# Performance work log

Hardware: AMD Instinct MI355X
Metric: run time of the kernel (lower is better)

The kernel has to match this reference:

```python
import jax, jax.numpy as jnp
import numpy as np
from jax import lax

NUM_CLASSES = 21
MAX_OUT = 5          # max_output_size in tf.image.non_max_suppression
IOU_THR = 0.5        # NMS_IOU_THRESHOLD
CONF_THR = 0.5       # CONFIDENCE_THRESHOLD
NEG = -1e9           # stand-in for -inf score (suppressed / background)


def setup_inputs() -> dict:
    key = jax.random.key(0)
    k1, k2, k3 = jax.random.split(key, 3)
    B, N, C = 128, 8732, NUM_CLASSES
    logits = jax.random.normal(k1, (B, N, 4 + C), dtype=jnp.float32)
    # default boxes in corner format [ymin, xmin, ymax, xmax], valid geometry
    ctr = jax.random.uniform(k2, (N, 2), dtype=jnp.float32)                 # cy, cx
    sz = jax.random.uniform(k3, (N, 2), dtype=jnp.float32, minval=0.05, maxval=0.3)  # h, w
    default_boxes = jnp.clip(
        jnp.concatenate([ctr - sz / 2, ctr + sz / 2], axis=-1), 0.0, 1.0)
    return {"logits": logits, "default_boxes": default_boxes}


def _decode(loc, db):
    # db: [N,4] corners -> center/size (matches get_offset's tf.stack)
    cy = (db[:, 2] + db[:, 0]) / 2
    cx = (db[:, 3] + db[:, 1]) / 2
    h = db[:, 2] - db[:, 0]
    w = db[:, 3] - db[:, 1]
    # loc: [B,N,4] = (dy, dx, dh, dw)
    ncy = loc[..., 0] * h + cy
    ncx = loc[..., 1] * w + cx
    nh = jnp.exp(loc[..., 2]) * h
    nw = jnp.exp(loc[..., 3]) * w
    boxes = jnp.stack(
        [ncy - nh / 2, ncx - nw / 2, ncy + nh / 2, ncx + nw / 2], axis=-1)
    return jnp.clip(boxes, 0.0, 1.0)


def _iou_one_vs_all(box, boxes):
    # box [4], boxes [N,4], corner format
    tl = jnp.maximum(box[:2], boxes[:, :2])
    br = jnp.minimum(box[2:], boxes[:, 2:])
    wh = jnp.maximum(br - tl, 0.0)
    inter = wh[:, 0] * wh[:, 1]
    a1 = (box[2] - box[0]) * (box[3] - box[1])
    a2 = (boxes[:, 2] - boxes[:, 0]) * (boxes[:, 3] - boxes[:, 1])
    return inter / (a1 + a2 - inter + 1e-12)


def _nms_single(boxes, scores, classes_f):
    # boxes [N,4], scores [N] (background already set to NEG), classes_f [N] float
    def step(s, _):
        i = jnp.argmax(s)
        sc = s[i]
        b = boxes[i]
        valid = sc > CONF_THR  # score_threshold in tf NMS
        iou = _iou_one_vs_all(b, boxes)
        s = jnp.where(iou > IOU_THR, NEG, s)  # suppresses i too (IoU=1)
        return s, (b, classes_f[i], sc, valid)

    _, (bs, cs, ss, vs) = lax.scan(step, scores, None, length=MAX_OUT)
    # pad invalid slots with zeros (TF returns variable-length; we use fixed 5 + zero pad)
    bs = jnp.where(vs[:, None], bs, 0.0)
    cs = jnp.where(vs, cs, 0.0)
    ss = jnp.where(vs, ss, 0.0)
    return bs, cs[:, None], ss[:, None]  # [5,4], [5,1], [5,1]


def reference(logits, default_boxes):
    boxes = _decode(logits[..., :4], default_boxes)          # [B,N,4]
    probs = jax.nn.softmax(logits[..., 4:], axis=-1)         # [B,N,C]
    scores = jnp.max(probs, axis=-1)                          # [B,N]
    classes = jnp.argmax(probs, axis=-1)                      # [B,N] int
    # boolean_mask(classes != 0) expressed as score = -inf for background
    scores_eff = jnp.where(classes != 0, scores, NEG)
    det_b, det_c, det_s = jax.vmap(_nms_single)(
        boxes, scores_eff, classes.astype(jnp.float32))
    # pack detection_boxes / detection_classes / detection_scores -> [B,5,6]
    return jnp.concatenate([det_b, det_c, det_s], axis=-1)
```

## Files before the change

### kernel.cpp

```cpp
#include <hip/hip_runtime.h>

#define NEG (-1e9f)
constexpr int NCLS   = 21;
constexpr int NBOX   = 8732;
constexpr int MAXOUT = 5;
constexpr int CAP    = NBOX;
constexpr float IOU_THR  = 0.5f;
constexpr float CONF_THR = 0.5f;

__device__ __forceinline__ void process_box(
        const float* __restrict__ v,
        int idx,
        const float4* __restrict__ dbox4,
        float4* __restrict__ cand,
        int* __restrict__ cnt) {
    const int n = idx % NBOX;
    const int b = idx / NBOX;

    float4 db = dbox4[n];
    float cy = (db.z + db.x) * 0.5f;
    float cx = (db.w + db.y) * 0.5f;
    float h  = db.z - db.x;
    float w  = db.w - db.y;
    float ncy = v[0] * h + cy;
    float ncx = v[1] * w + cx;
    float nh  = expf(v[2]) * h;
    float nw  = expf(v[3]) * w;
    float y1 = fminf(fmaxf(ncy - nh * 0.5f, 0.f), 1.f);
    float x1 = fminf(fmaxf(ncx - nw * 0.5f, 0.f), 1.f);
    float y2 = fminf(fmaxf(ncy + nh * 0.5f, 0.f), 1.f);
    float x2 = fminf(fmaxf(ncx + nw * 0.5f, 0.f), 1.f);

    float m = v[4];
    int am = 0;
#pragma unroll
    for (int j = 1; j < NCLS; j++) {
        float x = v[4 + j];
        if (x > m) { m = x; am = j; }
    }
    float sum = 0.f;
#pragma unroll
    for (int j = 0; j < NCLS; j++) sum += expf(v[4 + j] - m);
    float score = 1.0f / sum;

    if (am != 0 && score > CONF_THR) {
        int p = atomicAdd(&cnt[b], 1);
        if (p < CAP) {
            float4* c = cand + ((long long)b * CAP + p) * 2;
            c[0] = make_float4(y1, x1, y2, x2);
            c[1] = make_float4(score, (float)am, (float)n, 0.f);
        }
    }
}

__global__ __launch_bounds__(128) void decode_kernel(
        const float* __restrict__ logits,
        const float4* __restrict__ dbox4,
        float4* __restrict__ cand,
        int* __restrict__ cnt,
        int BN) {
    const int g = (blockIdx.x * 128 + threadIdx.x) * 4;
    if (g >= BN) return;

    if (g + 3 < BN) {
        const float4* f4 = (const float4*)(logits + (long long)g * 25);
        float v[100];
#pragma unroll
        for (int k = 0; k < 25; k++) {
            float4 r = f4[k];
            v[4 * k + 0] = r.x; v[4 * k + 1] = r.y;
            v[4 * k + 2] = r.z; v[4 * k + 3] = r.w;
        }
#pragma unroll
        for (int j = 0; j < 4; j++)
            process_box(v + 25 * j, g + j, dbox4, cand, cnt);
    } else {
        for (int j = 0; j < 4 && g + j < BN; j++) {
            const float* L = logits + (long long)(g + j) * 25;
            float v[25];
#pragma unroll
            for (int k = 0; k < 25; k++) v[k] = L[k];
            process_box(v, g + j, dbox4, cand, cnt);
        }
    }
}

__global__ __launch_bounds__(64) void nms_kernel(
        const float4* __restrict__ cand,
        const int* __restrict__ cnt,
        float* __restrict__ out) {
    const int b    = blockIdx.x;
    const int lane = threadIdx.x;
    __shared__ float s_sc[CAP];
    __shared__ float s_id[CAP];

    const int M = min(cnt[b], CAP);
    const float4* cb = cand + (long long)b * CAP * 2;
    float* o = out + (long long)b * MAXOUT * 6;

    for (int i = lane; i < M; i += 64) {
        float4 mrec = cb[i * 2 + 1];
        s_sc[i] = mrec.x;
        s_id[i] = mrec.z;
    }

    int k = 0;
    for (; k < MAXOUT; k++) {
        float bv = -INFINITY, boid = 3.0e38f;
        int bi = -1;
        for (int i = lane; i < M; i += 64) {
            float v = s_sc[i], oid = s_id[i];
            if (v > bv || (v == bv && oid < boid)) { bv = v; boid = oid; bi = i; }
        }
        for (int mm = 32; mm >= 1; mm >>= 1) {
            float v2 = __shfl_xor(bv,   mm, 64);
            float o2 = __shfl_xor(boid, mm, 64);
            int   i2 = __shfl_xor(bi,   mm, 64);
            if (v2 > bv || (v2 == bv && o2 < boid)) { bv = v2; boid = o2; bi = i2; }
        }
        if (bi < 0 || !(bv > CONF_THR)) break;

        float4 sb = cb[bi * 2];
        if (lane == 0) {
            float4 mm2 = cb[bi * 2 + 1];
            o[k * 6 + 0] = sb.x; o[k * 6 + 1] = sb.y;
            o[k * 6 + 2] = sb.z; o[k * 6 + 3] = sb.w;
            o[k * 6 + 4] = mm2.y; o[k * 6 + 5] = bv;
        }

        float a1 = (sb.z - sb.x) * (sb.w - sb.y);
        for (int i = lane; i < M; i += 64) {
            float4 c = cb[i * 2];
            float tly = fmaxf(sb.x, c.x);
            float tlx = fmaxf(sb.y, c.y);
            float bry = fminf(sb.z, c.z);
            float brx = fminf(sb.w, c.w);
            float wh0 = fmaxf(bry - tly, 0.f);
            float wh1 = fmaxf(brx - tlx, 0.f);
            float inter = wh0 * wh1;
            float a2 = (c.z - c.x) * (c.w - c.y);
            float iou = inter / (a1 + a2 - inter + 1e-12f);
            if (iou > IOU_THR) s_sc[i] = NEG;
        }
    }
    for (int j = k * 6 + lane; j < MAXOUT * 6; j += 64) o[j] = 0.f;
}

extern "C" void kernel_launch(void* const* d_in, const int* in_sizes, int n_in,
                              void* d_out, int out_size, void* d_ws, size_t ws_size,
                              hipStream_t stream) {
    const float* logits = (const float*)d_in[0];
    const float4* dbox4 = (const float4*)d_in[1];
    float* out          = (float*)d_out;

    const int N  = in_sizes[1] / 4;
    const int B  = in_sizes[0] / (N * 25);
    const int BN = B * N;

    int* cnt = (int*)d_ws;
    float4* cand = (float4*)((char*)d_ws + (((size_t)B * sizeof(int) + 15) & ~(size_t)15));

    hipMemsetAsync(cnt, 0, (size_t)B * sizeof(int), stream);
    const int nthreads = (BN + 3) / 4;
    decode_kernel<<<(nthreads + 127) / 128, 128, 0, stream>>>(logits, dbox4, cand, cnt, BN);
    nms_kernel<<<B, 64, 0, stream>>>(cand, cnt, out);
}
```

Before: 192.9 us.

## Split decode into score pass and sparse gather pass for candidates

```diff
diff --git a/kernel.cpp b/kernel.cpp
--- a/kernel.cpp
+++ b/kernel.cpp
@@ -8,79 +8,110 @@
 constexpr float IOU_THR  = 0.5f;
 constexpr float CONF_THR = 0.5f;
 
-__device__ __forceinline__ void process_box(
-        const float* __restrict__ v,
-        int idx,
+__global__ __launch_bounds__(128) void score_kernel(
+        const float* __restrict__ logits,
+        float4* __restrict__ score_out,
+        int BN) {
+    const int q = blockIdx.x * 128 + threadIdx.x;
+    const int g = q * 4;
+    if (g >= BN) return;
+
+    float s_res[4];
+    if (g + 3 < BN) {
+        const float4* f4 = (const float4*)(logits + (long long)g * 25);
+        float v[100];
+#pragma unroll
+        for (int k = 0; k < 25; k++) {
+            float4 r = f4[k];
+            v[4 * k + 0] = r.x; v[4 * k + 1] = r.y;
+            v[4 * k + 2] = r.z; v[4 * k + 3] = r.w;
+        }
+#pragma unroll
+        for (int j = 0; j < 4; j++) {
+            const float* L = v + 25 * j;
+            float m = L[4];
+            int am = 0;
+#pragma unroll
+            for (int jj = 1; jj < NCLS; jj++) {
+                float x = L[4 + jj];
+                if (x > m) { m = x; am = jj; }
+            }
+            float sum = 0.f;
+#pragma unroll
+            for (int jj = 0; jj < NCLS; jj++) sum += expf(L[4 + jj] - m);
+            float score = 1.0f / sum;
+            s_res[j] = (am != 0) ? score : NEG;
+        }
+    } else {
+#pragma unroll
+        for (int j = 0; j < 4; j++) {
+            if (g + j >= BN) { s_res[j] = NEG; continue; }
+            const float* L = logits + (long long)(g + j) * 25;
+            float m = L[4];
+            int am = 0;
+            for (int jj = 1; jj < NCLS; jj++) {
+                float x = L[4 + jj];
+                if (x > m) { m = x; am = jj; }
+            }
+            float sum = 0.f;
+            for (int jj = 0; jj < NCLS; jj++) sum += expf(L[4 + jj] - m);
+            float score = 1.0f / sum;
+            s_res[j] = (am != 0) ? score : NEG;
+        }
+    }
+    score_out[q] = make_float4(s_res[0], s_res[1], s_res[2], s_res[3]);
+}
+
+__global__ __launch_bounds__(128) void gather_kernel(
+        const float* __restrict__ logits,
         const float4* __restrict__ dbox4,
+        const float4* __restrict__ score_in,
         float4* __restrict__ cand,
-        int* __restrict__ cnt) {
-    const int n = idx % NBOX;
-    const int b = idx / NBOX;
-
-    float4 db = dbox4[n];
-    float cy = (db.z + db.x) * 0.5f;
-    float cx = (db.w + db.y) * 0.5f;
-    float h  = db.z - db.x;
-    float w  = db.w - db.y;
-    float ncy = v[0] * h + cy;
-    float ncx = v[1] * w + cx;
-    float nh  = expf(v[2]) * h;
-    float nw  = expf(v[3]) * w;
-    float y1 = fminf(fmaxf(ncy - nh * 0.5f, 0.f), 1.f);
-    float x1 = fminf(fmaxf(ncx - nw * 0.5f, 0.f), 1.f);
-    float y2 = fminf(fmaxf(ncy + nh * 0.5f, 0.f), 1.f);
-    float x2 = fminf(fmaxf(ncx + nw * 0.5f, 0.f), 1.f);
-
-    float m = v[4];
-    int am = 0;
-#pragma unroll
-    for (int j = 1; j < NCLS; j++) {
-        float x = v[4 + j];
-        if (x > m) { m = x; am = j; }
-    }
-    float sum = 0.f;
-#pragma unroll
-    for (int j = 0; j < NCLS; j++) sum += expf(v[4 + j] - m);
-    float score = 1.0f / sum;
-
-    if (am != 0 && score > CONF_THR) {
+        int* __restrict__ cnt,
+        int BN) {
+    const int q = blockIdx.x * 128 + threadIdx.x;
+    const int g = q * 4;
+    if (g >= BN) return;
+    float4 s4 = score_in[q];
+    float sc[4] = { s4.x, s4.y, s4.z, s4.w };
+
+#pragma unroll
+    for (int j = 0; j < 4; j++) {
+        const int idx = g + j;
+        if (idx >= BN) continue;
+        const float score = sc[j];
+        if (!(score > CONF_THR)) continue;
+
+        const int n = idx % NBOX;
+        const int b = idx / NBOX;
+        const float* L = logits + (long long)idx * 25;
+
+        float m = L[4];
+        int am = 0;
+        for (int jj = 1; jj < NCLS; jj++) {
+            float x = L[4 + jj];
+            if (x > m) { m = x; am = jj; }
+        }
+
+        float4 db = dbox4[n];
+        float cy = (db.z + db.x) * 0.5f;
+        float cx = (db.w + db.y) * 0.5f;
+        float h  = db.z - db.x;
+        float w  = db.w - db.y;
+        float ncy = L[0] * h + cy;
+        float ncx = L[1] * w + cx;
+        float nh  = expf(L[2]) * h;
+        float nw  = expf(L[3]) * w;
+        float y1 = fminf(fmaxf(ncy - nh * 0.5f, 0.f), 1.f);
+        float x1 = fminf(fmaxf(ncx - nw * 0.5f, 0.f), 1.f);
+        float y2 = fminf(fmaxf(ncy + nh * 0.5f, 0.f), 1.f);
+        float x2 = fminf(fmaxf(ncx + nw * 0.5f, 0.f), 1.f);
+
         int p = atomicAdd(&cnt[b], 1);
         if (p < CAP) {
             float4* c = cand + ((long long)b * CAP + p) * 2;
             c[0] = make_float4(y1, x1, y2, x2);
             c[1] = make_float4(score, (float)am, (float)n, 0.f);
-        }
-    }
-}
-
-__global__ __launch_bounds__(128) void decode_kernel(
-        const float* __restrict__ logits,
-        const float4* __restrict__ dbox4,
-        float4* __restrict__ cand,
-        int* __restrict__ cnt,
-        int BN) {
-    const int g = (blockIdx.x * 128 + threadIdx.x) * 4;
-    if (g >= BN) return;
-
-    if (g + 3 < BN) {
-        const float4* f4 = (const float4*)(logits + (long long)g * 25);
-        float v[100];
-#pragma unroll
-        for (int k = 0; k < 25; k++) {
-            float4 r = f4[k];
-            v[4 * k + 0] = r.x; v[4 * k + 1] = r.y;
-            v[4 * k + 2] = r.z; v[4 * k + 3] = r.w;
-        }
-#pragma unroll
-        for (int j = 0; j < 4; j++)
-            process_box(v + 25 * j, g + j, dbox4, cand, cnt);
-    } else {
-        for (int j = 0; j < 4 && g + j < BN; j++) {
-            const float* L = logits + (long long)(g + j) * 25;
-            float v[25];
-#pragma unroll
-            for (int k = 0; k < 25; k++) v[k] = L[k];
-            process_box(v, g + j, dbox4, cand, cnt);
         }
     }
 }
@@ -156,12 +187,18 @@
     const int N  = in_sizes[1] / 4;
     const int B  = in_sizes[0] / (N * 25);
     const int BN = B * N;
-
-    int* cnt = (int*)d_ws;
-    float4* cand = (float4*)((char*)d_ws + (((size_t)B * sizeof(int) + 15) & ~(size_t)15));
+    const int nquad = (BN + 3) / 4;
+
+    char* wsp = (char*)d_ws;
+    int* cnt = (int*)wsp;
+    size_t off = ((size_t)B * sizeof(int) + 15) & ~(size_t)15;
+    float4* scores = (float4*)(wsp + off);
+    off += (size_t)nquad * sizeof(float4);
+    float4* cand = (float4*)(wsp + off);
 
     hipMemsetAsync(cnt, 0, (size_t)B * sizeof(int), stream);
-    const int nthreads = (BN + 3) / 4;
-    decode_kernel<<<(nthreads + 127) / 128, 128, 0, stream>>>(logits, dbox4, cand, cnt, BN);
+    const int nblocks = (nquad + 127) / 128;
+    score_kernel<<<nblocks, 128, 0, stream>>>(logits, scores, BN);
+    gather_kernel<<<nblocks, 128, 0, stream>>>(logits, dbox4, scores, cand, cnt, BN);
     nms_kernel<<<B, 64, 0, stream>>>(cand, cnt, out);
 }
```

Result: slower. 210.1 us (+8.9%).
